# Kernel optimization log

Hardware: AMD Instinct MI355X
Metric: run time of the kernel (lower is better)

## Reference

```python
import jax, jax.numpy as jnp
import numpy as np

HEADS = 8
DIM_HEAD = 40
QUERY_DIM = 320
N_OBJS = 8
HW = 64  # 64x64 latent -> w_h = 4096
N = HW * HW + 4 * N_OBJS  # 4128 visual + grounding tokens


def _build_keep_mask(att_masks):
    # att_masks: [B, O, 64, 64] binary instance masks
    B, O, h, w = att_masks.shape
    W = h * w
    m = att_masks.reshape(B, O, W)                      # [B, O, W]
    # per-object outer products summed over objects (bmm in torch)
    ind = jnp.einsum('bow,bov->bwv', m, m)              # [B, W, W]
    # torch sets visual[ind<1]=0 then visual[ind>=1]=1 -> pure threshold
    visual = (ind >= 1.0).astype(m.dtype)               # [B, W, W]
    # with the middle 2 blocks (rows O:3O) forced to 1
    bl = jnp.tile(m, (1, 4, 1))                         # [B, 4O, W]
    bl = bl.at[:, O:3 * O, :].set(1.0)
    tr = jnp.swapaxes(bl, 1, 2)                         # [B, W, 4O]
    n = W + 4 * O
    top = jnp.concatenate([visual, tr], axis=2)         # [B, W, N]
    bot = jnp.concatenate([bl, jnp.ones((B, 4 * O, 4 * O), m.dtype)], axis=2)
    full = jnp.concatenate([top, bot], axis=1)          # [B, N, N]
    full = full + jnp.eye(n, dtype=m.dtype) * 1e-9      # diagonal epsilon
    return full > 0.0                                   # keep where > 0


def setup_inputs() -> dict:
    key = jax.random.key(0)
    ks = jax.random.split(key, 7)
    B = 1
    x = jax.random.normal(ks[0], (B, N, QUERY_DIM), jnp.float32)
    att_masks = (jax.random.uniform(ks[1], (B, N_OBJS, HW, HW)) < 0.15).astype(jnp.float32)
    inner = HEADS * DIM_HEAD
    s = QUERY_DIM ** -0.5
    Wq = jax.random.normal(ks[2], (QUERY_DIM, inner), jnp.float32) * s
    Wk = jax.random.normal(ks[3], (QUERY_DIM, inner), jnp.float32) * s
    Wv = jax.random.normal(ks[4], (QUERY_DIM, inner), jnp.float32) * s
    Wo = jax.random.normal(ks[5], (inner, QUERY_DIM), jnp.float32) * (inner ** -0.5)
    bo = jnp.zeros((QUERY_DIM,), jnp.float32)
    return {"x": x, "att_masks": att_masks, "Wq": Wq, "Wk": Wk, "Wv": Wv, "Wo": Wo, "bo": bo}


def reference(x, att_masks, Wq, Wk, Wv, Wo, bo):
    B, n, _ = x.shape
    q = (x @ Wq).reshape(B, n, HEADS, DIM_HEAD)
    k = (x @ Wk).reshape(B, n, HEADS, DIM_HEAD)
    v = (x @ Wv).reshape(B, n, HEADS, DIM_HEAD)
    sim = jnp.einsum('bihc,bjhc->bhij', q, k) * (DIM_HEAD ** -0.5)  # [B,H,N,N]
    keep = _build_keep_mask(att_masks)                              # [B,N,N]
    sim = jnp.where(keep[:, None, :, :], sim, -jnp.inf)
    attn = jax.nn.softmax(sim, axis=-1)
    out = jnp.einsum('bhij,bjhc->bihc', attn, v).reshape(B, n, HEADS * DIM_HEAD)
    return out @ Wo + bo
```

## Files before the change

### kernel.cpp

```cpp
#include <hip/hip_runtime.h>

typedef __bf16 bf16;
using short8 = __attribute__((ext_vector_type(8))) __bf16;
using f32x4  = __attribute__((ext_vector_type(4))) float;

#define N_TOK 4128
#define QD    320
#define DH    40
#define W_VIS 4096
#define SPLITS 8
#define N_SP  4224
#define BSTRIDE 344

#if __has_builtin(__builtin_amdgcn_exp2f)
#define EXP2F(x) __builtin_amdgcn_exp2f(x)
#else
#define EXP2F(x) exp2f(x)
#endif

__device__ __forceinline__ float loadS(const void* b, long i, bool isbf) {
  return isbf ? (float)((const bf16*)b)[i] : ((const float*)b)[i];
}
__device__ __forceinline__ unsigned short bfbits(float x) {
  bf16 h = (bf16)x;
  return __builtin_bit_cast(unsigned short, h);
}

__device__ __forceinline__ bool blk_sniff(const unsigned short* att_h, int nthr) {
  __shared__ int s;
  if (threadIdx.x == 0) s = 0;
  __syncthreads();
  int step = 8192 / nthr;
  if (att_h[threadIdx.x * step] != 0) atomicOr(&s, 1);
  __syncthreads();
  return s != 0;
}

__device__ __forceinline__ short8 load_afrag(const void* x, long row, int koff, bool isbf) {
  if (isbf) return *(const short8*)((const bf16*)x + row * QD + koff);
  const float* f = (const float*)x + row * QD + koff;
  float4 a = *(const float4*)f, b = *(const float4*)(f + 4);
  union { short8 v; unsigned short e[8]; } u;
  u.e[0] = bfbits(a.x); u.e[1] = bfbits(a.y); u.e[2] = bfbits(a.z); u.e[3] = bfbits(a.w);
  u.e[4] = bfbits(b.x); u.e[5] = bfbits(b.y); u.e[6] = bfbits(b.z); u.e[7] = bfbits(b.w);
  return u.v;
}

__global__ __launch_bounds__(256) void qkv_mega(
    const void* __restrict__ x, const void* __restrict__ att,
    const void* __restrict__ Wq, const void* __restrict__ Wk, const void* __restrict__ Wv,
    bf16* __restrict__ q, bf16* __restrict__ kswz, bf16* __restrict__ vswz,
    unsigned short* __restrict__ awA, unsigned short* __restrict__ bwB) {
  bool isbf = blk_sniff((const unsigned short*)att, 256);
  if (blockIdx.y == 15) {
    int flat = blockIdx.x * 256 + threadIdx.x;
    if (flat < N_SP) {
      int t = flat;
      unsigned int Aw = 0u, Bw = 0u;
      if (t < N_TOK) {
        unsigned int b9 = 0u; bool forced = false;
        if (t < W_VIS) {
#pragma unroll
          for (int o = 0; o < 8; ++o)
            if (loadS(att, o * W_VIS + t, isbf) != 0.0f) b9 |= (1u << o);
        } else {
          int g = t - W_VIS;
          int rep = g >> 3, oo = g & 7;
          forced = (rep == 1 || rep == 2);
          b9 = 0x100u | (forced ? 0u : (1u << oo));
        }
        Aw = b9 | (forced ? 0x200u : 0u) | 0x400u;
        Bw = b9 | (forced ? 0x400u : 0u) | 0x200u;
      }
      awA[t] = (unsigned short)Aw;
      bwB[t] = (unsigned short)Bw;
    } else if (flat - N_SP < 8320) {
      int idx = flat - N_SP;
#pragma unroll
      for (int m = 0; m < 4; ++m) {
        int t = idx * 4 + m;
        int li8 = t & 7; int t2 = t >> 3;
        int q2 = t2 & 3; t2 >>= 2;
        int ksv = t2 & 1; t2 >>= 1;
        int kt = t2 % 65, h = t2 / 65;
        bf16 val = (li8 == 0) ? (bf16)1.0f : (bf16)0.0f;
        short8 v8 = {val, val, val, val, val, val, val, val};
        long base = (((long)h * 65 + kt) * 6 + ksv * 3 + 2) * 512;
        *(short8*)(vswz + base + (q2 * 16 + 8 + li8) * 8) = v8;
      }
    }
    return;
  }
  __shared__ unsigned short lbuf[64 * BSTRIDE];
  int m0 = blockIdx.x * 64;
  int ng = blockIdx.y * 64;
  int wsel = ng / 320;
  int n_in = ng % 320;
  const void* W = wsel == 0 ? Wq : wsel == 1 ? Wk : Wv;
  {
    int krow0 = threadIdx.x >> 2;
    int c16 = (threadIdx.x & 3) * 16;
#pragma unroll
    for (int it = 0; it < 5; ++it) {
      int kk = it * 64 + krow0;
      if (!isbf) {
        const float* wp = (const float*)W + (long)kk * QD + n_in + c16;
        float4 f0 = *(const float4*)wp,     f1 = *(const float4*)(wp + 4);
        float4 f2 = *(const float4*)(wp + 8), f3 = *(const float4*)(wp + 12);
        float fv[16] = {f0.x, f0.y, f0.z, f0.w, f1.x, f1.y, f1.z, f1.w,
                        f2.x, f2.y, f2.z, f2.w, f3.x, f3.y, f3.z, f3.w};
#pragma unroll
        for (int j = 0; j < 16; ++j) lbuf[(c16 + j) * BSTRIDE + kk] = bfbits(fv[j]);
      } else {
        const unsigned short* wp = (const unsigned short*)W + (long)kk * QD + n_in + c16;
#pragma unroll
        for (int j4 = 0; j4 < 4; ++j4) {
          ushort4 u4 = *(const ushort4*)(wp + j4 * 4);
          lbuf[(c16 + j4 * 4 + 0) * BSTRIDE + kk] = u4.x;
          lbuf[(c16 + j4 * 4 + 1) * BSTRIDE + kk] = u4.y;
          lbuf[(c16 + j4 * 4 + 2) * BSTRIDE + kk] = u4.z;
          lbuf[(c16 + j4 * 4 + 3) * BSTRIDE + kk] = u4.w;
        }
      }
    }
  }
  __syncthreads();
  int wv = threadIdx.x >> 6, lane = threadIdx.x & 63;
  int quad = lane >> 4, li = lane & 15;
  int wm = wv >> 1, wn = wv & 1;
  f32x4 acc[2][2];
#pragma unroll
  for (int a = 0; a < 2; a++)
#pragma unroll
    for (int b = 0; b < 2; b++) acc[a][b] = (f32x4){0.f, 0.f, 0.f, 0.f};
#pragma unroll
  for (int ks = 0; ks < 10; ++ks) {
    short8 af[2], bfrag[2];
#pragma unroll
    for (int mt = 0; mt < 2; ++mt) {
      long r = m0 + wm * 32 + mt * 16 + li;
      if (r > N_TOK - 1) r = N_TOK - 1;
      af[mt] = load_afrag(x, r, ks * 32 + quad * 8, isbf);
    }
#pragma unroll
    for (int nt = 0; nt < 2; ++nt) {
      int nr = wn * 32 + nt * 16 + li;
      bfrag[nt] = *(const short8*)&lbuf[nr * BSTRIDE + ks * 32 + quad * 8];
    }
#pragma unroll
    for (int mt = 0; mt < 2; ++mt)
#pragma unroll
      for (int nt = 0; nt < 2; ++nt)
        acc[mt][nt] = __builtin_amdgcn_mfma_f32_16x16x32_bf16(af[mt], bfrag[nt], acc[mt][nt], 0, 0, 0);
  }
  __syncthreads();
  unsigned short (*ct)[68] = (unsigned short(*)[68])lbuf;
  const float qs = (wsel == 0) ? 0.15811388300841898f * 1.4426950408889634f : 1.0f;
#pragma unroll
  for (int mt = 0; mt < 2; ++mt)
#pragma unroll
    for (int nt = 0; nt < 2; ++nt)
#pragma unroll
      for (int r = 0; r < 4; ++r)
        ct[wm * 32 + mt * 16 + quad * 4 + r][wn * 32 + nt * 16 + li] =
            bfbits(acc[mt][nt][r] * qs);
  __syncthreads();
  int kt = m0 >> 6;
  if (wsel == 0) {
    int row = threadIdx.x >> 2, c4 = threadIdx.x & 3;
    int grow = m0 + row;
    if (grow < N_TOK) {
#pragma unroll
      for (int i = 0; i < 4; ++i) {
        int cg = c4 + i * 4;
        int col = n_in + cg * 4;
        int h = col / DH, d = col % DH;
        ushort4 pk = *(const ushort4*)&ct[row][cg * 4];
        *(ushort4*)(q + (long)h * N_TOK * DH + (long)grow * DH + d) = pk;
      }
    }
  } else if (wsel == 1) {
#pragma unroll
    for (int rep = 0; rep < 2; ++rep) {
      int u = threadIdx.x + rep * 256;
      int row = u >> 3, c8 = (u & 7) * 8;
      int gcol = n_in + c8;
      int h = gcol / DH, d0 = gcol % DH;
      int li2 = row & 15, nt2 = row >> 4;
      long base = (((long)h * 65 + kt) * 4 + nt2) * 640 +
                  (d0 < 32 ? ((d0 >> 3) * 16 + li2) * 8 : 512 + li2 * 8);
      ushort4 a = *(const ushort4*)&ct[row][c8];
      ushort4 b = *(const ushort4*)&ct[row][c8 + 4];
      *(ushort4*)(kswz + base) = a;
      *(ushort4*)(kswz + base + 4) = b;
    }
  } else {
#pragma unroll
    for (int rep = 0; rep < 2; ++rep) {
      int u = threadIdx.x + rep * 256;
      int g = u & 7, dcol = u >> 3;
      int gcol = n_in + dcol;
      int h = gcol / DH, d = gcol % DH;
      int dt = d >> 4, li2 = d & 15, ksv = g >> 2, q2 = g & 3;
      union { unsigned short e[8]; ushort4 v[2]; } o;
#pragma unroll
      for (int j = 0; j < 8; ++j) o.e[j] = ct[g * 8 + j][dcol];
      long base = (((long)h * 65 + kt) * 6 + ksv * 3 + dt) * 512 + (q2 * 16 + li2) * 8;
      *(ushort4*)(vswz + base) = o.v[0];
      *(ushort4*)(vswz + base + 4) = o.v[1];
    }
  }
}

__global__ __launch_bounds__(256, 3) void attn_kernel(
    const bf16* __restrict__ qg, const bf16* __restrict__ kswz, const bf16* __restrict__ vswz,
    const unsigned short* __restrict__ awA, const unsigned short* __restrict__ bwB,
    float* __restrict__ opart, float* __restrict__ lpart) {
  __shared__ unsigned short pbuf[4][32][68];
  int bid = blockIdx.x;
  int h = bid & 7;
  int sp = (bid >> 3) & 7;
  int qt = bid >> 6;
  int kt0 = (sp * 65) >> 3;
  int kt1 = ((sp + 1) * 65) >> 3;
  int wv = threadIdx.x >> 6, lane = threadIdx.x & 63;
  int quad = lane >> 4, li = lane & 15;
  const bf16* qh = qg + h * (N_TOK * DH);
  const bf16* kz = kswz + (long)h * 65 * 2560;
  const bf16* vz = vswz + (long)h * 65 * 3072;

  int qrow_base = qt * 128 + wv * 32;
  short8 qa0[2], qa1[2];
  unsigned int aw[2][4]; int qi[2][4];
#pragma unroll
  for (int mt = 0; mt < 2; ++mt) {
    int qr = qrow_base + mt * 16 + li; if (qr > N_TOK - 1) qr = N_TOK - 1;
    qa0[mt] = *(const short8*)(qh + qr * DH + quad * 8);
    qa1[mt] = (quad == 0) ? *(const short8*)(qh + qr * DH + 32) : (short8)(__bf16)0.0f;
#pragma unroll
    for (int r = 0; r < 4; ++r) {
      qi[mt][r] = qrow_base + mt * 16 + quad * 4 + r;
      aw[mt][r] = awA[qi[mt][r]];
    }
  }

  f32x4 o[2][3];
#pragma unroll
  for (int mt = 0; mt < 2; ++mt)
#pragma unroll
    for (int d = 0; d < 3; ++d) o[mt][d] = (f32x4){0.f, 0.f, 0.f, 0.f};
  const f32x4 cm8 = (f32x4){-8.f, -8.f, -8.f, -8.f};
  int dkt = qrow_base >> 6;

  for (int kt = kt0; kt < kt1; ++kt) {
    const bf16* kb_base = kz + (long)kt * 2560;
    f32x4 s[2][4];
    unsigned int bw[4];
#pragma unroll
    for (int nt = 0; nt < 4; ++nt) {
      bw[nt] = bwB[kt * 64 + nt * 16 + li];
      short8 kb0 = *(const short8*)(kb_base + nt * 640 + lane * 8);
      short8 kb1 = (quad == 0) ? *(const short8*)(kb_base + nt * 640 + 512 + li * 8)
                               : (short8)(__bf16)0.0f;
      s[0][nt] = __builtin_amdgcn_mfma_f32_16x16x32_bf16(qa0[0], kb0, cm8, 0, 0, 0);
      s[0][nt] = __builtin_amdgcn_mfma_f32_16x16x32_bf16(qa1[0], kb1, s[0][nt], 0, 0, 0);
      s[1][nt] = __builtin_amdgcn_mfma_f32_16x16x32_bf16(qa0[1], kb0, cm8, 0, 0, 0);
      s[1][nt] = __builtin_amdgcn_mfma_f32_16x16x32_bf16(qa1[1], kb1, s[1][nt], 0, 0, 0);
    }
    short8 vb[2][3];
#pragma unroll
    for (int ksv = 0; ksv < 2; ++ksv)
#pragma unroll
      for (int dt = 0; dt < 3; ++dt)
        vb[ksv][dt] = *(const short8*)(vz + ((long)kt * 6 + ksv * 3 + dt) * 512 + lane * 8);
    if (kt == dkt) {
#pragma unroll
      for (int mt = 0; mt < 2; ++mt)
#pragma unroll
        for (int nt = 0; nt < 4; ++nt)
#pragma unroll
          for (int r = 0; r < 4; ++r) {
            bool kp = ((aw[mt][r] & bw[nt]) != 0u) ||
                      (qi[mt][r] == (kt * 64 + nt * 16 + li));
            float p = EXP2F(kp ? s[mt][nt][r] : -1e5f);
            pbuf[wv][mt * 16 + quad * 4 + r][nt * 16 + li] =
                (unsigned short)(__builtin_bit_cast(unsigned int, p) >> 16);
          }
    } else {
#pragma unroll
      for (int mt = 0; mt < 2; ++mt)
#pragma unroll
        for (int nt = 0; nt < 4; ++nt)
#pragma unroll
          for (int r = 0; r < 4; ++r) {
            bool kp = (aw[mt][r] & bw[nt]) != 0u;
            float p = EXP2F(kp ? s[mt][nt][r] : -1e5f);
            pbuf[wv][mt * 16 + quad * 4 + r][nt * 16 + li] =
                (unsigned short)(__builtin_bit_cast(unsigned int, p) >> 16);
          }
    }
#pragma unroll
    for (int ksv = 0; ksv < 2; ++ksv) {
      union { short8 v; ushort4 u[2]; } fp[2];
#pragma unroll
      for (int mt = 0; mt < 2; ++mt) {
        fp[mt].u[0] = *(const ushort4*)&pbuf[wv][mt * 16 + li][ksv * 32 + quad * 8];
        fp[mt].u[1] = *(const ushort4*)&pbuf[wv][mt * 16 + li][ksv * 32 + quad * 8 + 4];
      }
#pragma unroll
      for (int dt = 0; dt < 3; ++dt) {
        o[0][dt] = __builtin_amdgcn_mfma_f32_16x16x32_bf16(fp[0].v, vb[ksv][dt], o[0][dt], 0, 0, 0);
        o[1][dt] = __builtin_amdgcn_mfma_f32_16x16x32_bf16(fp[1].v, vb[ksv][dt], o[1][dt], 0, 0, 0);
      }
    }
  }
  long pb2 = (long)(sp * 8 + h) * N_SP;
#pragma unroll
  for (int mt = 0; mt < 2; ++mt) {
#pragma unroll
    for (int dt = 0; dt < 3; ++dt) {
      int d = dt * 16 + li;
      if (d < DH) {
#pragma unroll
        for (int r = 0; r < 4; ++r)
          opart[(pb2 + qi[mt][r]) * DH + d] = o[mt][dt][r];
      }
    }
    if (li == 8) {
#pragma unroll
      for (int r = 0; r < 4; ++r) lpart[pb2 + qi[mt][r]] = o[mt][2][r];
    }
  }
}

__global__ __launch_bounds__(256) void combine_kernel(
    const float* __restrict__ opart, const float* __restrict__ lpart,
    bf16* __restrict__ attn) {
  int id = blockIdx.x * 256 + threadIdx.x;
  if (id >= 8 * N_TOK * 10) return;
  int d4 = id % 10;
  int rw = (id / 10) % N_TOK;
  int h = id / (10 * N_TOK);
  float4 osum = make_float4(0.f, 0.f, 0.f, 0.f);
  float lsum = 0.f;
#pragma unroll
  for (int s = 0; s < SPLITS; ++s) {
    long rb = (long)(s * 8 + h) * N_SP + rw;
    float4 ov = *(const float4*)(opart + rb * DH + d4 * 4);
    osum.x += ov.x; osum.y += ov.y; osum.z += ov.z; osum.w += ov.w;
    lsum += lpart[rb];
  }
  float rl = 1.0f / fmaxf(lsum, 1e-30f);
  union { short4 s4; unsigned short hh[4]; } u;
  u.hh[0] = bfbits(osum.x * rl); u.hh[1] = bfbits(osum.y * rl);
  u.hh[2] = bfbits(osum.z * rl); u.hh[3] = bfbits(osum.w * rl);
  *(short4*)(attn + rw * QD + h * DH + d4 * 4) = u.s4;
}

__global__ __launch_bounds__(256) void gemm_out(
    const bf16* __restrict__ A, const void* __restrict__ Wo,
    const void* __restrict__ bias, const void* __restrict__ att,
    void* __restrict__ out) {
  bool isbf = blk_sniff((const unsigned short*)att, 256);
  __shared__ unsigned short lbuf[64 * BSTRIDE];
  int m0 = blockIdx.x * 64;
  int n0 = blockIdx.y * 64;
  {
    int krow0 = threadIdx.x >> 2;
    int c16 = (threadIdx.x & 3) * 16;
#pragma unroll
    for (int it = 0; it < 5; ++it) {
      int kk = it * 64 + krow0;
      if (!isbf) {
        const float* wp = (const float*)Wo + (long)kk * QD + n0 + c16;
        float4 f0 = *(const float4*)wp,     f1 = *(const float4*)(wp + 4);
        float4 f2 = *(const float4*)(wp + 8), f3 = *(const float4*)(wp + 12);
        float fv[16] = {f0.x, f0.y, f0.z, f0.w, f1.x, f1.y, f1.z, f1.w,
                        f2.x, f2.y, f2.z, f2.w, f3.x, f3.y, f3.z, f3.w};
#pragma unroll
        for (int j = 0; j < 16; ++j) lbuf[(c16 + j) * BSTRIDE + kk] = bfbits(fv[j]);
      } else {
        const unsigned short* wp = (const unsigned short*)Wo + (long)kk * QD + n0 + c16;
#pragma unroll
        for (int j4 = 0; j4 < 4; ++j4) {
          ushort4 u4 = *(const ushort4*)(wp + j4 * 4);
          lbuf[(c16 + j4 * 4 + 0) * BSTRIDE + kk] = u4.x;
          lbuf[(c16 + j4 * 4 + 1) * BSTRIDE + kk] = u4.y;
          lbuf[(c16 + j4 * 4 + 2) * BSTRIDE + kk] = u4.z;
          lbuf[(c16 + j4 * 4 + 3) * BSTRIDE + kk] = u4.w;
        }
      }
    }
  }
  __syncthreads();
  int wv = threadIdx.x >> 6, lane = threadIdx.x & 63;
  int quad = lane >> 4, li = lane & 15;
  int wm = wv >> 1, wn = wv & 1;
  f32x4 acc[2][2];
#pragma unroll
  for (int a = 0; a < 2; a++)
#pragma unroll
    for (int b = 0; b < 2; b++) acc[a][b] = (f32x4){0.f, 0.f, 0.f, 0.f};
#pragma unroll
  for (int ks = 0; ks < 10; ++ks) {
    short8 af[2], bfrag[2];
#pragma unroll
    for (int mt = 0; mt < 2; ++mt) {
      int r = m0 + wm * 32 + mt * 16 + li;
      r = r < N_TOK ? r : N_TOK - 1;
      af[mt] = *(const short8*)(A + r * QD + ks * 32 + quad * 8);
    }
#pragma unroll
    for (int nt = 0; nt < 2; ++nt) {
      int nr = wn * 32 + nt * 16 + li;
      bfrag[nt] = *(const short8*)&lbuf[nr * BSTRIDE + ks * 32 + quad * 8];
    }
#pragma unroll
    for (int mt = 0; mt < 2; ++mt)
#pragma unroll
      for (int nt = 0; nt < 2; ++nt)
        acc[mt][nt] = __builtin_amdgcn_mfma_f32_16x16x32_bf16(af[mt], bfrag[nt], acc[mt][nt], 0, 0, 0);
  }
#pragma unroll
  for (int mt = 0; mt < 2; ++mt)
#pragma unroll
    for (int nt = 0; nt < 2; ++nt)
#pragma unroll
      for (int r = 0; r < 4; ++r) {
        int row = m0 + wm * 32 + mt * 16 + quad * 4 + r;
        if (row >= N_TOK) continue;
        int col = n0 + wn * 32 + nt * 16 + li;
        float val = acc[mt][nt][r] + loadS(bias, col, isbf);
        if (isbf) ((bf16*)out)[row * QD + col] = (bf16)val;
        else      ((float*)out)[row * QD + col] = val;
      }
}

extern "C" void kernel_launch(void* const* d_in, const int* in_sizes, int n_in,
                              void* d_out, int out_size, void* d_ws, size_t ws_size,
                              hipStream_t stream) {
  (void)in_sizes; (void)n_in; (void)out_size; (void)ws_size;
  const void* x   = d_in[0];
  const void* att = d_in[1];
  const void* Wq  = d_in[2];
  const void* Wk  = d_in[3];
  const void* Wv  = d_in[4];
  const void* Wo  = d_in[5];
  const void* bo  = d_in[6];
  char* ws = (char*)d_ws;
  unsigned short* awA = (unsigned short*)(ws + 0);
  unsigned short* bwB = (unsigned short*)(ws + 8704);
  bf16* qb    = (bf16*)(ws + 17408);
  bf16* kswz  = (bf16*)(ws + 2659328);
  bf16* vswz  = (bf16*)(ws + 5321728);
  bf16* attnb = (bf16*)(ws + 8516608);
  float* opart = (float*)(ws + 11158528);
  float* lpart = (float*)(ws + 54412288);

  dim3 g1(65, 16);
  qkv_mega<<<g1, 256, 0, stream>>>(x, att, Wq, Wk, Wv, qb, kswz, vswz, awA, bwB);
  attn_kernel<<<33 * SPLITS * 8, 256, 0, stream>>>(qb, kswz, vswz, awA, bwB, opart, lpart);
  combine_kernel<<<(8 * N_TOK * 10 + 255) / 256, 256, 0, stream>>>(opart, lpart, attnb);
  dim3 g2(65, 5);
  gemm_out<<<g2, 256, 0, stream>>>(attnb, Wo, bo, att, d_out);
}
```

Measured before the change: 177.4 us.

## Compute attention mask via extra MFMA on bf16 mask embeddings

Replaces the per-element bitwise mask test (awA & bwB) with an extra MFMA that dots bf16-encoded mask features of queries and keys. The result is combined with the scores through fminf, so masked entries get a large negative value before exp2. It also transposes the score MFMA so each lane holds contiguous columns, packs pairs of bf16 probabilities into a swizzled uint LDS buffer for wider stores and loads, and shrinks the partial-row padding. This adds MFMA work and mask-fragment loads per tile, in exchange for removing scalar ALU mask logic and scattered 16-bit LDS stores.

New measurement: 205.2 us. +15.7%, slower.

```diff
diff --git a/kernel.cpp b/kernel.cpp
--- a/kernel.cpp
+++ b/kernel.cpp
@@ -10,6 +10,7 @@
 #define W_VIS 4096
 #define SPLITS 8
 #define N_SP  4224
+#define PROWS 4160
 #define BSTRIDE 344
 
 #if __has_builtin(__builtin_amdgcn_exp2f)
@@ -50,30 +51,50 @@
     const void* __restrict__ x, const void* __restrict__ att,
     const void* __restrict__ Wq, const void* __restrict__ Wk, const void* __restrict__ Wv,
     bf16* __restrict__ q, bf16* __restrict__ kswz, bf16* __restrict__ vswz,
-    unsigned short* __restrict__ awA, unsigned short* __restrict__ bwB) {
+    bf16* __restrict__ maskKz, bf16* __restrict__ maskQb) {
   bool isbf = blk_sniff((const unsigned short*)att, 256);
   if (blockIdx.y == 15) {
     int flat = blockIdx.x * 256 + threadIdx.x;
     if (flat < N_SP) {
       int t = flat;
-      unsigned int Aw = 0u, Bw = 0u;
-      if (t < N_TOK) {
-        unsigned int b9 = 0u; bool forced = false;
-        if (t < W_VIS) {
-#pragma unroll
-          for (int o = 0; o < 8; ++o)
-            if (loadS(att, o * W_VIS + t, isbf) != 0.0f) b9 |= (1u << o);
-        } else {
-          int g = t - W_VIS;
-          int rep = g >> 3, oo = g & 7;
-          forced = (rep == 1 || rep == 2);
-          b9 = 0x100u | (forced ? 0u : (1u << oo));
-        }
-        Aw = b9 | (forced ? 0x200u : 0u) | 0x400u;
-        Bw = b9 | (forced ? 0x400u : 0u) | 0x200u;
-      }
-      awA[t] = (unsigned short)Aw;
-      bwB[t] = (unsigned short)Bw;
+      unsigned int bits = 0u; bool ground = false, forced = false;
+      bool realt = t < N_TOK;
+      if (t < W_VIS) {
+#pragma unroll
+        for (int o = 0; o < 8; ++o)
+          if (loadS(att, o * W_VIS + t, isbf) != 0.0f) bits |= (1u << o);
+      } else if (realt) {
+        int g = t - W_VIS;
+        int rep = g >> 3, oo = g & 7;
+        ground = true; forced = (rep == 1 || rep == 2);
+        if (!forced) bits = 1u << oo;
+      }
+      const unsigned short PB = bfbits(200.0f), NB = bfbits(-200.0f), ONE = bfbits(1.0f);
+      union { short8 v; unsigned short e[8]; } w;
+      short8 zz = (short8)(__bf16)0.0f;
+      long tb = (long)(t >> 4) * 64 + (t & 15);
+#pragma unroll
+      for (int j = 0; j < 8; ++j) w.e[j] = ((bits >> j) & 1u) ? PB : (unsigned short)0;
+      *(short8*)(maskQb + (tb + 0) * 8) = w.v;
+      w.e[0] = ground ? PB : (unsigned short)0;
+      w.e[1] = forced ? PB : (unsigned short)0;
+      w.e[2] = realt ? PB : (unsigned short)0;
+      w.e[3] = NB; w.e[4] = 0; w.e[5] = 0; w.e[6] = 0; w.e[7] = 0;
+      *(short8*)(maskQb + (tb + 16) * 8) = w.v;
+      *(short8*)(maskQb + (tb + 32) * 8) = zz;
+      *(short8*)(maskQb + (tb + 48) * 8) = zz;
+      if (t < PROWS) {
+#pragma unroll
+        for (int j = 0; j < 8; ++j) w.e[j] = ((bits >> j) & 1u) ? ONE : (unsigned short)0;
+        *(short8*)(maskKz + (tb + 0) * 8) = w.v;
+        w.e[0] = ground ? ONE : (unsigned short)0;
+        w.e[1] = realt ? ONE : (unsigned short)0;
+        w.e[2] = forced ? ONE : (unsigned short)0;
+        w.e[3] = ONE; w.e[4] = 0; w.e[5] = 0; w.e[6] = 0; w.e[7] = 0;
+        *(short8*)(maskKz + (tb + 16) * 8) = w.v;
+        *(short8*)(maskKz + (tb + 32) * 8) = zz;
+        *(short8*)(maskKz + (tb + 48) * 8) = zz;
+      }
     } else if (flat - N_SP < 8320) {
       int idx = flat - N_SP;
 #pragma unroll
@@ -212,11 +233,32 @@
   }
 }
 
+#define SOFTMAX_PHASE(DIAG)                                                    \
+  _Pragma("unroll")                                                            \
+  for (int mt = 0; mt < 2; ++mt) {                                             \
+    _Pragma("unroll")                                                          \
+    for (int nt = 0; nt < 4; ++nt) {                                           \
+      float e[4];                                                              \
+      _Pragma("unroll")                                                        \
+      for (int r = 0; r < 4; ++r) {                                            \
+        float pm = fminf(s[mt][nt][r], s2[mt][nt][r]);                         \
+        if (DIAG) pm = (dlhs == ((nt - mt) * 16 + r)) ? s[mt][nt][r] : pm;     \
+        e[r] = EXP2F(pm);                                                      \
+      }                                                                        \
+      unsigned int u0 = (__builtin_bit_cast(unsigned int, e[0]) >> 16) |       \
+                        (__builtin_bit_cast(unsigned int, e[1]) & 0xffff0000u);\
+      unsigned int u1 = (__builtin_bit_cast(unsigned int, e[2]) >> 16) |       \
+                        (__builtin_bit_cast(unsigned int, e[3]) & 0xffff0000u);\
+      int pc = (nt * 8 + quad * 2) ^ swz;                                      \
+      *(uint2*)&pbuf[wv][mt * 16 + li][pc] = make_uint2(u0, u1);               \
+    }                                                                          \
+  }
+
 __global__ __launch_bounds__(256, 3) void attn_kernel(
     const bf16* __restrict__ qg, const bf16* __restrict__ kswz, const bf16* __restrict__ vswz,
-    const unsigned short* __restrict__ awA, const unsigned short* __restrict__ bwB,
+    const bf16* __restrict__ maskKz, const bf16* __restrict__ maskQb,
     float* __restrict__ opart, float* __restrict__ lpart) {
-  __shared__ unsigned short pbuf[4][32][68];
+  __shared__ __align__(16) unsigned int pbuf[4][32][32];
   int bid = blockIdx.x;
   int h = bid & 7;
   int sp = (bid >> 3) & 7;
@@ -230,18 +272,14 @@
   const bf16* vz = vswz + (long)h * 65 * 3072;
 
   int qrow_base = qt * 128 + wv * 32;
-  short8 qa0[2], qa1[2];
-  unsigned int aw[2][4]; int qi[2][4];
+  short8 qa0[2], qa1[2], qmb[2];
 #pragma unroll
   for (int mt = 0; mt < 2; ++mt) {
     int qr = qrow_base + mt * 16 + li; if (qr > N_TOK - 1) qr = N_TOK - 1;
     qa0[mt] = *(const short8*)(qh + qr * DH + quad * 8);
     qa1[mt] = (quad == 0) ? *(const short8*)(qh + qr * DH + 32) : (short8)(__bf16)0.0f;
-#pragma unroll
-    for (int r = 0; r < 4; ++r) {
-      qi[mt][r] = qrow_base + mt * 16 + quad * 4 + r;
-      aw[mt][r] = awA[qi[mt][r]];
-    }
+    qmb[mt] = *(const short8*)(maskQb +
+                 ((long)((qrow_base >> 4) + mt) * 64 + quad * 16 + li) * 8);
   }
 
   f32x4 o[2][3];
@@ -251,21 +289,25 @@
     for (int d = 0; d < 3; ++d) o[mt][d] = (f32x4){0.f, 0.f, 0.f, 0.f};
   const f32x4 cm8 = (f32x4){-8.f, -8.f, -8.f, -8.f};
   int dkt = qrow_base >> 6;
+  int dlhs = li - quad * 4 + (qrow_base & 63);
+  int swz = (li & 7) << 2;
 
   for (int kt = kt0; kt < kt1; ++kt) {
     const bf16* kb_base = kz + (long)kt * 2560;
-    f32x4 s[2][4];
-    unsigned int bw[4];
+    const bf16* mk_base = maskKz + (long)kt * 2048;
+    f32x4 s[2][4], s2[2][4];
 #pragma unroll
     for (int nt = 0; nt < 4; ++nt) {
-      bw[nt] = bwB[kt * 64 + nt * 16 + li];
       short8 kb0 = *(const short8*)(kb_base + nt * 640 + lane * 8);
       short8 kb1 = (quad == 0) ? *(const short8*)(kb_base + nt * 640 + 512 + li * 8)
                                : (short8)(__bf16)0.0f;
-      s[0][nt] = __builtin_amdgcn_mfma_f32_16x16x32_bf16(qa0[0], kb0, cm8, 0, 0, 0);
-      s[0][nt] = __builtin_amdgcn_mfma_f32_16x16x32_bf16(qa1[0], kb1, s[0][nt], 0, 0, 0);
-      s[1][nt] = __builtin_amdgcn_mfma_f32_16x16x32_bf16(qa0[1], kb0, cm8, 0, 0, 0);
-      s[1][nt] = __builtin_amdgcn_mfma_f32_16x16x32_bf16(qa1[1], kb1, s[1][nt], 0, 0, 0);
+      short8 amf = *(const short8*)(mk_base + ((long)nt * 64 + quad * 16 + li) * 8);
+      s[0][nt] = __builtin_amdgcn_mfma_f32_16x16x32_bf16(kb0, qa0[0], cm8, 0, 0, 0);
+      s[0][nt] = __builtin_amdgcn_mfma_f32_16x16x32_bf16(kb1, qa1[0], s[0][nt], 0, 0, 0);
+      s2[0][nt] = __builtin_amdgcn_mfma_f32_16x16x32_bf16(amf, qmb[0], s[0][nt], 0, 0, 0);
+      s[1][nt] = __builtin_amdgcn_mfma_f32_16x16x32_bf16(kb0, qa0[1], cm8, 0, 0, 0);
+      s[1][nt] = __builtin_amdgcn_mfma_f32_16x16x32_bf16(kb1, qa1[1], s[1][nt], 0, 0, 0);
+      s2[1][nt] = __builtin_amdgcn_mfma_f32_16x16x32_bf16(amf, qmb[1], s[1][nt], 0, 0, 0);
     }
     short8 vb[2][3];
 #pragma unroll
@@ -274,39 +316,16 @@
       for (int dt = 0; dt < 3; ++dt)
         vb[ksv][dt] = *(const short8*)(vz + ((long)kt * 6 + ksv * 3 + dt) * 512 + lane * 8);
     if (kt == dkt) {
-#pragma unroll
-      for (int mt = 0; mt < 2; ++mt)
-#pragma unroll
-        for (int nt = 0; nt < 4; ++nt)
-#pragma unroll
-          for (int r = 0; r < 4; ++r) {
-            bool kp = ((aw[mt][r] & bw[nt]) != 0u) ||
-                      (qi[mt][r] == (kt * 64 + nt * 16 + li));
-            float p = EXP2F(kp ? s[mt][nt][r] : -1e5f);
-            pbuf[wv][mt * 16 + quad * 4 + r][nt * 16 + li] =
-                (unsigned short)(__builtin_bit_cast(unsigned int, p) >> 16);
-          }
+      SOFTMAX_PHASE(true)
     } else {
-#pragma unroll
-      for (int mt = 0; mt < 2; ++mt)
-#pragma unroll
-        for (int nt = 0; nt < 4; ++nt)
-#pragma unroll
-          for (int r = 0; r < 4; ++r) {
-            bool kp = (aw[mt][r] & bw[nt]) != 0u;
-            float p = EXP2F(kp ? s[mt][nt][r] : -1e5f);
-            pbuf[wv][mt * 16 + quad * 4 + r][nt * 16 + li] =
-                (unsigned short)(__builtin_bit_cast(unsigned int, p) >> 16);
-          }
+      SOFTMAX_PHASE(false)
     }
 #pragma unroll
     for (int ksv = 0; ksv < 2; ++ksv) {
-      union { short8 v; ushort4 u[2]; } fp[2];
-#pragma unroll
-      for (int mt = 0; mt < 2; ++mt) {
-        fp[mt].u[0] = *(const ushort4*)&pbuf[wv][mt * 16 + li][ksv * 32 + quad * 8];
-        fp[mt].u[1] = *(const ushort4*)&pbuf[wv][mt * 16 + li][ksv * 32 + quad * 8 + 4];
-      }
+      union { uint4 u; short8 v; } fp[2];
+      int rc = (ksv * 16 + quad * 4) ^ swz;
+      fp[0].u = *(const uint4*)&pbuf[wv][li][rc];
+      fp[1].u = *(const uint4*)&pbuf[wv][16 + li][rc];
 #pragma unroll
       for (int dt = 0; dt < 3; ++dt) {
         o[0][dt] = __builtin_amdgcn_mfma_f32_16x16x32_bf16(fp[0].v, vb[ksv][dt], o[0][dt], 0, 0, 0);
@@ -314,7 +333,7 @@
       }
     }
   }
-  long pb2 = (long)(sp * 8 + h) * N_SP;
+  long pb2 = (long)(sp * 8 + h) * PROWS;
 #pragma unroll
   for (int mt = 0; mt < 2; ++mt) {
 #pragma unroll
@@ -322,13 +341,18 @@
       int d = dt * 16 + li;
       if (d < DH) {
 #pragma unroll
-        for (int r = 0; r < 4; ++r)
-          opart[(pb2 + qi[mt][r]) * DH + d] = o[mt][dt][r];
+        for (int r = 0; r < 4; ++r) {
+          int qi = qrow_base + mt * 16 + quad * 4 + r;
+          if (qi < PROWS) opart[(pb2 + qi) * DH + d] = o[mt][dt][r];
+        }
       }
     }
     if (li == 8) {
 #pragma unroll
-      for (int r = 0; r < 4; ++r) lpart[pb2 + qi[mt][r]] = o[mt][2][r];
+      for (int r = 0; r < 4; ++r) {
+        int qi = qrow_base + mt * 16 + quad * 4 + r;
+        if (qi < PROWS) lpart[pb2 + qi] = o[mt][2][r];
+      }
     }
   }
 }
@@ -345,7 +369,7 @@
   float lsum = 0.f;
 #pragma unroll
   for (int s = 0; s < SPLITS; ++s) {
-    long rb = (long)(s * 8 + h) * N_SP + rw;
+    long rb = (long)(s * 8 + h) * PROWS + rw;
     float4 ov = *(const float4*)(opart + rb * DH + d4 * 4);
     osum.x += ov.x; osum.y += ov.y; osum.z += ov.z; osum.w += ov.w;
     lsum += lpart[rb];
@@ -448,18 +472,18 @@
   const void* Wo  = d_in[5];
   const void* bo  = d_in[6];
   char* ws = (char*)d_ws;
-  unsigned short* awA = (unsigned short*)(ws + 0);
-  unsigned short* bwB = (unsigned short*)(ws + 8704);
-  bf16* qb    = (bf16*)(ws + 17408);
-  bf16* kswz  = (bf16*)(ws + 2659328);
-  bf16* vswz  = (bf16*)(ws + 5321728);
-  bf16* attnb = (bf16*)(ws + 8516608);
-  float* opart = (float*)(ws + 11158528);
-  float* lpart = (float*)(ws + 54412288);
+  bf16* maskQb = (bf16*)(ws + 0);
+  bf16* maskKz = (bf16*)(ws + 270336);
+  bf16* qb     = (bf16*)(ws + 536576);
+  bf16* kswz   = (bf16*)(ws + 3178496);
+  bf16* vswz   = (bf16*)(ws + 5840896);
+  bf16* attnb  = (bf16*)(ws + 9035776);
+  float* opart = (float*)(ws + 11677696);
+  float* lpart = (float*)(ws + 54276096);
 
   dim3 g1(65, 16);
-  qkv_mega<<<g1, 256, 0, stream>>>(x, att, Wq, Wk, Wv, qb, kswz, vswz, awA, bwB);
-  attn_kernel<<<33 * SPLITS * 8, 256, 0, stream>>>(qb, kswz, vswz, awA, bwB, opart, lpart);
+  qkv_mega<<<g1, 256, 0, stream>>>(x, att, Wq, Wk, Wv, qb, kswz, vswz, maskKz, maskQb);
+  attn_kernel<<<33 * SPLITS * 8, 256, 0, stream>>>(qb, kswz, vswz, maskKz, maskQb, opart, lpart);
   combine_kernel<<<(8 * N_TOK * 10 + 255) / 256, 256, 0, stream>>>(opart, lpart, attnb);
   dim3 g2(65, 5);
   gemm_out<<<g2, 256, 0, stream>>>(attnb, Wo, bo, att, d_out);
```

## Double-buffer K tile loads in registers and relax launch bounds to two waves

Applied to the files above, without the earlier changes.

Splits the attention loop into a K-load helper and a compute body, then unrolls the loop by two and ping-pongs between two register sets. The next tile's K and mask words are fetched while the current tile is computed, hiding global load latency behind the QK and PV MFMAs. Launch bounds drop from 3 to 2 blocks per CU to make room for the extra registers, which lowers occupancy and with it some latency hiding across waves.

Measured after the change: 179.9 us. Within noise of the previous version (+1.4%).

```diff
diff --git a/kernel.cpp b/kernel.cpp
--- a/kernel.cpp
+++ b/kernel.cpp
@@ -212,7 +212,84 @@
   }
 }
 
-__global__ __launch_bounds__(256, 3) void attn_kernel(
+__device__ __forceinline__ void attn_loadk(
+    int kt, int lane, int quad, int li,
+    const bf16* __restrict__ kz, const unsigned short* __restrict__ bwB,
+    short8 (&kb0)[4], short8 (&kb1)[4], unsigned int (&bw)[4]) {
+  const bf16* kbp = kz + (long)kt * 2560;
+#pragma unroll
+  for (int nt = 0; nt < 4; ++nt) {
+    bw[nt] = bwB[kt * 64 + nt * 16 + li];
+    kb0[nt] = *(const short8*)(kbp + nt * 640 + lane * 8);
+    kb1[nt] = (quad == 0) ? *(const short8*)(kbp + nt * 640 + 512 + li * 8)
+                          : (short8)(__bf16)0.0f;
+  }
+}
+
+__device__ __forceinline__ void attn_body(
+    int kt, int dkt, int quad, int li, int lane,
+    const short8 (&qa0)[2], const short8 (&qa1)[2],
+    const unsigned int (&aw)[2][4], const int (&qi)[2][4],
+    const short8 (&kb0)[4], const short8 (&kb1)[4], const unsigned int (&bw)[4],
+    const bf16* __restrict__ vz, f32x4 (&o)[2][3], unsigned short (*pb)[68]) {
+  const f32x4 cm8 = (f32x4){-8.f, -8.f, -8.f, -8.f};
+  f32x4 s[2][4];
+#pragma unroll
+  for (int nt = 0; nt < 4; ++nt) {
+    s[0][nt] = __builtin_amdgcn_mfma_f32_16x16x32_bf16(qa0[0], kb0[nt], cm8, 0, 0, 0);
+    s[0][nt] = __builtin_amdgcn_mfma_f32_16x16x32_bf16(qa1[0], kb1[nt], s[0][nt], 0, 0, 0);
+    s[1][nt] = __builtin_amdgcn_mfma_f32_16x16x32_bf16(qa0[1], kb0[nt], cm8, 0, 0, 0);
+    s[1][nt] = __builtin_amdgcn_mfma_f32_16x16x32_bf16(qa1[1], kb1[nt], s[1][nt], 0, 0, 0);
+  }
+  short8 vb[2][3];
+#pragma unroll
+  for (int ksv = 0; ksv < 2; ++ksv)
+#pragma unroll
+    for (int dt = 0; dt < 3; ++dt)
+      vb[ksv][dt] = *(const short8*)(vz + ((long)kt * 6 + ksv * 3 + dt) * 512 + lane * 8);
+  if (kt == dkt) {
+#pragma unroll
+    for (int mt = 0; mt < 2; ++mt)
+#pragma unroll
+      for (int nt = 0; nt < 4; ++nt)
+#pragma unroll
+        for (int r = 0; r < 4; ++r) {
+          bool kp = ((aw[mt][r] & bw[nt]) != 0u) ||
+                    (qi[mt][r] == (kt * 64 + nt * 16 + li));
+          float p = EXP2F(kp ? s[mt][nt][r] : -1e5f);
+          pb[mt * 16 + quad * 4 + r][nt * 16 + li] =
+              (unsigned short)(__builtin_bit_cast(unsigned int, p) >> 16);
+        }
+  } else {
+#pragma unroll
+    for (int mt = 0; mt < 2; ++mt)
+#pragma unroll
+      for (int nt = 0; nt < 4; ++nt)
+#pragma unroll
+        for (int r = 0; r < 4; ++r) {
+          bool kp = (aw[mt][r] & bw[nt]) != 0u;
+          float p = EXP2F(kp ? s[mt][nt][r] : -1e5f);
+          pb[mt * 16 + quad * 4 + r][nt * 16 + li] =
+              (unsigned short)(__builtin_bit_cast(unsigned int, p) >> 16);
+        }
+  }
+#pragma unroll
+  for (int ksv = 0; ksv < 2; ++ksv) {
+    union { short8 v; ushort4 u[2]; } fp[2];
+#pragma unroll
+    for (int mt = 0; mt < 2; ++mt) {
+      fp[mt].u[0] = *(const ushort4*)&pb[mt * 16 + li][ksv * 32 + quad * 8];
+      fp[mt].u[1] = *(const ushort4*)&pb[mt * 16 + li][ksv * 32 + quad * 8 + 4];
+    }
+#pragma unroll
+    for (int dt = 0; dt < 3; ++dt) {
+      o[0][dt] = __builtin_amdgcn_mfma_f32_16x16x32_bf16(fp[0].v, vb[ksv][dt], o[0][dt], 0, 0, 0);
+      o[1][dt] = __builtin_amdgcn_mfma_f32_16x16x32_bf16(fp[1].v, vb[ksv][dt], o[1][dt], 0, 0, 0);
+    }
+  }
+}
+
+__global__ __launch_bounds__(256, 2) void attn_kernel(
     const bf16* __restrict__ qg, const bf16* __restrict__ kswz, const bf16* __restrict__ vswz,
     const unsigned short* __restrict__ awA, const unsigned short* __restrict__ bwB,
     float* __restrict__ opart, float* __restrict__ lpart) {
@@ -249,71 +326,22 @@
   for (int mt = 0; mt < 2; ++mt)
 #pragma unroll
     for (int d = 0; d < 3; ++d) o[mt][d] = (f32x4){0.f, 0.f, 0.f, 0.f};
-  const f32x4 cm8 = (f32x4){-8.f, -8.f, -8.f, -8.f};
   int dkt = qrow_base >> 6;
 
-  for (int kt = kt0; kt < kt1; ++kt) {
-    const bf16* kb_base = kz + (long)kt * 2560;
-    f32x4 s[2][4];
-    unsigned int bw[4];
-#pragma unroll
-    for (int nt = 0; nt < 4; ++nt) {
-      bw[nt] = bwB[kt * 64 + nt * 16 + li];
-      short8 kb0 = *(const short8*)(kb_base + nt * 640 + lane * 8);
-      short8 kb1 = (quad == 0) ? *(const short8*)(kb_base + nt * 640 + 512 + li * 8)
-                               : (short8)(__bf16)0.0f;
-      s[0][nt] = __builtin_amdgcn_mfma_f32_16x16x32_bf16(qa0[0], kb0, cm8, 0, 0, 0);
-      s[0][nt] = __builtin_amdgcn_mfma_f32_16x16x32_bf16(qa1[0], kb1, s[0][nt], 0, 0, 0);
-      s[1][nt] = __builtin_amdgcn_mfma_f32_16x16x32_bf16(qa0[1], kb0, cm8, 0, 0, 0);
-      s[1][nt] = __builtin_amdgcn_mfma_f32_16x16x32_bf16(qa1[1], kb1, s[1][nt], 0, 0, 0);
-    }
-    short8 vb[2][3];
-#pragma unroll
-    for (int ksv = 0; ksv < 2; ++ksv)
-#pragma unroll
-      for (int dt = 0; dt < 3; ++dt)
-        vb[ksv][dt] = *(const short8*)(vz + ((long)kt * 6 + ksv * 3 + dt) * 512 + lane * 8);
-    if (kt == dkt) {
-#pragma unroll
-      for (int mt = 0; mt < 2; ++mt)
-#pragma unroll
-        for (int nt = 0; nt < 4; ++nt)
-#pragma unroll
-          for (int r = 0; r < 4; ++r) {
-            bool kp = ((aw[mt][r] & bw[nt]) != 0u) ||
-                      (qi[mt][r] == (kt * 64 + nt * 16 + li));
-            float p = EXP2F(kp ? s[mt][nt][r] : -1e5f);
-            pbuf[wv][mt * 16 + quad * 4 + r][nt * 16 + li] =
-                (unsigned short)(__builtin_bit_cast(unsigned int, p) >> 16);
-          }
-    } else {
-#pragma unroll
-      for (int mt = 0; mt < 2; ++mt)
-#pragma unroll
-        for (int nt = 0; nt < 4; ++nt)
-#pragma unroll
-          for (int r = 0; r < 4; ++r) {
-            bool kp = (aw[mt][r] & bw[nt]) != 0u;
-            float p = EXP2F(kp ? s[mt][nt][r] : -1e5f);
-            pbuf[wv][mt * 16 + quad * 4 + r][nt * 16 + li] =
-                (unsigned short)(__builtin_bit_cast(unsigned int, p) >> 16);
-          }
-    }
-#pragma unroll
-    for (int ksv = 0; ksv < 2; ++ksv) {
-      union { short8 v; ushort4 u[2]; } fp[2];
-#pragma unroll
-      for (int mt = 0; mt < 2; ++mt) {
-        fp[mt].u[0] = *(const ushort4*)&pbuf[wv][mt * 16 + li][ksv * 32 + quad * 8];
-        fp[mt].u[1] = *(const ushort4*)&pbuf[wv][mt * 16 + li][ksv * 32 + quad * 8 + 4];
-      }
-#pragma unroll
-      for (int dt = 0; dt < 3; ++dt) {
-        o[0][dt] = __builtin_amdgcn_mfma_f32_16x16x32_bf16(fp[0].v, vb[ksv][dt], o[0][dt], 0, 0, 0);
-        o[1][dt] = __builtin_amdgcn_mfma_f32_16x16x32_bf16(fp[1].v, vb[ksv][dt], o[1][dt], 0, 0, 0);
-      }
-    }
-  }
+  short8 kb0A[4], kb1A[4], kb0B[4], kb1B[4];
+  unsigned int bwA[4], bwBr[4];
+  int kt = kt0;
+  attn_loadk(kt, lane, quad, li, kz, bwB, kb0A, kb1A, bwA);
+  for (; kt + 2 <= kt1; kt += 2) {
+    attn_loadk(kt + 1, lane, quad, li, kz, bwB, kb0B, kb1B, bwBr);
+    attn_body(kt, dkt, quad, li, lane, qa0, qa1, aw, qi, kb0A, kb1A, bwA, vz, o, pbuf[wv]);
+    if (kt + 2 < kt1)
+      attn_loadk(kt + 2, lane, quad, li, kz, bwB, kb0A, kb1A, bwA);
+    attn_body(kt + 1, dkt, quad, li, lane, qa0, qa1, aw, qi, kb0B, kb1B, bwBr, vz, o, pbuf[wv]);
+  }
+  if (kt < kt1)
+    attn_body(kt, dkt, quad, li, lane, qa0, qa1, aw, qi, kb0A, kb1A, bwA, vz, o, pbuf[wv]);
+
   long pb2 = (long)(sp * 8 + h) * N_SP;
 #pragma unroll
   for (int mt = 0; mt < 2; ++mt) {
```
